# Kernel tuning notes

Hardware: AMD Instinct MI355X
Metric: run time of the kernel (lower is better)

Reference implementation:

```python
import jax, jax.numpy as jnp
import numpy as np

NUM_GRAPHS = 1024


def _mlp2(h, Wa, ba, Wb, bb):
    # Linear -> ReLU -> Linear
    return jax.nn.relu(h @ Wa + ba) @ Wb + bb


def setup_inputs() -> dict:
    key = jax.random.key(0)
    ks = jax.random.split(key, 16)
    N, F, H, C, E = 100000, 128, 128, 10, 1600000
    x = jax.random.normal(ks[0], (N, F), dtype=jnp.float32)
    edge_index = jax.random.randint(ks[1], (2, E), 0, N, dtype=jnp.int64)
    batch = jnp.sort(jax.random.randint(ks[2], (N,), 0, NUM_GRAPHS, dtype=jnp.int64))
    s = 1.0 / np.sqrt(H)
    def w(k, shape):
        return jax.random.uniform(k, shape, jnp.float32, -s, s)
    return {
        "x": x, "edge_index": edge_index, "batch": batch,
        "W1a": w(ks[3], (F, H)), "b1a": w(ks[4], (H,)),
        "W1b": w(ks[5], (H, H)), "b1b": w(ks[6], (H,)),
        "W2a": w(ks[7], (H, H)), "b2a": w(ks[8], (H,)),
        "W2b": w(ks[9], (H, H)), "b2b": w(ks[10], (H,)),
        "Wl1": w(ks[11], (H, H)), "bl1": w(ks[12], (H,)),
        "Wl2": w(ks[13], (H, C)), "bl2": w(ks[14], (C,)),
    }


def reference(x, edge_index, batch, W1a, b1a, W1b, b1b, W2a, b2a, W2b, b2b, Wl1, bl1, Wl2, bl2):
    N = x.shape[0]
    src, dst = edge_index[0], edge_index[1]

    def gin_conv(h, Wa, ba, Wb, bb):
        # sum-aggregate neighbor features: agg[i] = sum_{(src->dst=i)} h[src]
        agg = jax.ops.segment_sum(h[src], dst, num_segments=N)
        # eps = 0 (PyG default): nn((1+eps)*h + agg)
        return _mlp2(h + agg, Wa, ba, Wb, bb)

    h = jax.nn.relu(gin_conv(x, W1a, b1a, W1b, b1b))
    h = jax.nn.relu(gin_conv(h, W2a, b2a, W2b, b2b))
    # global_add_pool over graph ids -> [num_graphs, H]
    g = jax.ops.segment_sum(h, batch, num_segments=NUM_GRAPHS)
    g = jax.nn.relu(g @ Wl1 + bl1)
    return jax.nn.log_softmax(g @ Wl2 + bl2, axis=1)
```

## Files before the change

kernel.cpp:

```cpp
#include <hip/hip_runtime.h>
#include <hip/hip_bf16.h>
#include <math.h>

#define NUM_GRAPHS 1024

typedef __attribute__((ext_vector_type(8))) short bf16x8;
typedef __attribute__((ext_vector_type(4))) float f32x4;

static __device__ __forceinline__ unsigned short f2bf(float f) {
    union { float f; unsigned u; } v; v.f = f;
    unsigned r = v.u + 0x7fffu + ((v.u >> 16) & 1u);
    return (unsigned short)(r >> 16);
}
static __device__ __forceinline__ float bf_lo(unsigned u) { return __uint_as_float(u << 16); }
static __device__ __forceinline__ float bf_hi(unsigned u) { return __uint_as_float(u & 0xffff0000u); }

__global__ void k_pre(const int* __restrict__ eiDst, int E,
                      int* __restrict__ deg, int* __restrict__ rank,
                      const float* __restrict__ x, int n4, unsigned* __restrict__ xb,
                      float* __restrict__ G, int eb) {
    if ((int)blockIdx.x < eb) {
        int e = blockIdx.x * 256 + threadIdx.x;
        if (e < E) rank[e] = atomicAdd(&deg[eiDst[e]], 1);
    } else if ((int)blockIdx.x < eb + 4096) {
        int i = (blockIdx.x - eb) * 256 + threadIdx.x;
        int stride = 4096 * 256;
        const float4* x4 = (const float4*)x;
        for (; i < n4; i += stride) {
            float4 v = x4[i];
            unsigned lo = (unsigned)f2bf(v.x) | ((unsigned)f2bf(v.y) << 16);
            unsigned hi = (unsigned)f2bf(v.z) | ((unsigned)f2bf(v.w) << 16);
            ((uint2*)xb)[i] = make_uint2(lo, hi);
        }
    } else {
        int i = (blockIdx.x - eb - 4096) * 256 + threadIdx.x;
        float4* G4 = (float4*)G;
        for (; i < NUM_GRAPHS * 32; i += 64 * 256)
            G4[i] = make_float4(0.f, 0.f, 0.f, 0.f);
    }
}

__global__ void k_scan1(const int* __restrict__ deg, int N,
                        int* __restrict__ excl, int* __restrict__ bsum) {
    __shared__ int s[256];
    int i = blockIdx.x * 256 + threadIdx.x;
    int v = (i < N) ? deg[i] : 0;
    s[threadIdx.x] = v;
    __syncthreads();
    for (int off = 1; off < 256; off <<= 1) {
        int t = (threadIdx.x >= off) ? s[threadIdx.x - off] : 0;
        __syncthreads();
        s[threadIdx.x] += t;
        __syncthreads();
    }
    if (i < N) excl[i] = s[threadIdx.x] - v;
    if (threadIdx.x == 255) bsum[blockIdx.x] = s[255];
}

__global__ void k_scan23(const int* __restrict__ excl, const int* __restrict__ bsum,
                         int nb, int N, int E, int* __restrict__ rp) {
    __shared__ int s[512];
    const int t = threadIdx.x;
    for (int k = t; k < 512; k += 256) s[k] = (k < nb) ? bsum[k] : 0;
    __syncthreads();
    #pragma unroll
    for (int off = 1; off < 512; off <<= 1) {
        int a = (t >= off) ? s[t - off] : 0;
        int b = s[t + 256 - off];
        __syncthreads();
        s[t] += a;
        s[t + 256] += b;
        __syncthreads();
    }
    const int myIncl = s[blockIdx.x];
    const int myOwn = bsum[blockIdx.x];
    const int off_b = myIncl - myOwn;
    int i = blockIdx.x * 256 + t;
    if (i < N) rp[i] = excl[i] + off_b;
    if (i == 0) rp[N] = E;
}

#define FILL_PASSES 3
#define FILL_RANGE 33334
#define FILL_BLOCKS 2048
__global__ void k_fillprep(const int* __restrict__ ei, const int* __restrict__ rank,
                           int E, const int* __restrict__ rp, int* __restrict__ srcs,
                           const float* __restrict__ W0, const float* __restrict__ W1,
                           const float* __restrict__ W2, const float* __restrict__ W3,
                           unsigned short* __restrict__ wt) {
    if ((int)blockIdx.x < FILL_BLOCKS) {
        const int tid0 = blockIdx.x * 256 + threadIdx.x;
        const int stride = FILL_BLOCKS * 256;
        for (int pass = 0; pass < FILL_PASSES; ++pass) {
            const int lo = pass * FILL_RANGE;
            const int hi = lo + FILL_RANGE;
            for (int e = tid0; e < E; e += stride) {
                int d = ei[(size_t)E + e];
                if (d >= lo && d < hi) {
                    srcs[rp[d] + rank[e]] = ei[e];
                }
            }
        }
    } else {
        int lb = blockIdx.x - FILL_BLOCKS;
        int b = lb >> 6;
        const float* W = (b == 0) ? W0 : (b == 1) ? W1 : (b == 2) ? W2 : W3;
        int idx = (lb & 63) * 256 + threadIdx.x;
        int k = idx >> 7, n = idx & 127;
        wt[b * 16384 + n * 128 + k] = f2bf(W[idx]);
    }
}

__device__ __forceinline__ void acc8(float* a, uint4 v) {
    a[0] += bf_lo(v.x); a[1] += bf_hi(v.x);
    a[2] += bf_lo(v.y); a[3] += bf_hi(v.y);
    a[4] += bf_lo(v.z); a[5] += bf_hi(v.z);
    a[6] += bf_lo(v.w); a[7] += bf_hi(v.w);
}

__global__ __launch_bounds__(256, 8)
void k_aggq(const uint4* __restrict__ H4, const int* __restrict__ rp,
            const int* __restrict__ srcs, int N, uint4* __restrict__ out) {
    int gw = (blockIdx.x * blockDim.x + threadIdx.x) >> 6;
    int lane = threadIdx.x & 63;
    int q = lane >> 4, ql = lane & 15;
    int n = gw * 4 + q;
    if (gw * 4 >= N) return;
    bool act = (n < N);
    int nc = act ? n : 0;
    uint4 s0 = H4[(size_t)nc * 16 + ql];
    float a[8];
    a[0] = bf_lo(s0.x); a[1] = bf_hi(s0.x);
    a[2] = bf_lo(s0.y); a[3] = bf_hi(s0.y);
    a[4] = bf_lo(s0.z); a[5] = bf_hi(s0.z);
    a[6] = bf_lo(s0.w); a[7] = bf_hi(s0.w);
    int j = act ? rp[nc] : 0;
    int e = act ? rp[nc + 1] : 0;
    while (j + 4 <= e) {
        int i0 = srcs[j], i1 = srcs[j + 1], i2 = srcs[j + 2], i3 = srcs[j + 3];
        uint4 v0 = H4[(size_t)i0 * 16 + ql];
        uint4 v1 = H4[(size_t)i1 * 16 + ql];
        uint4 v2 = H4[(size_t)i2 * 16 + ql];
        uint4 v3 = H4[(size_t)i3 * 16 + ql];
        acc8(a, v0); acc8(a, v1); acc8(a, v2); acc8(a, v3);
        j += 4;
    }
    while (j < e) {
        uint4 v = H4[(size_t)srcs[j] * 16 + ql];
        acc8(a, v);
        ++j;
    }
    if (act) {
        uint4 o;
        o.x = (unsigned)f2bf(a[0]) | ((unsigned)f2bf(a[1]) << 16);
        o.y = (unsigned)f2bf(a[2]) | ((unsigned)f2bf(a[3]) << 16);
        o.z = (unsigned)f2bf(a[4]) | ((unsigned)f2bf(a[5]) << 16);
        o.w = (unsigned)f2bf(a[6]) | ((unsigned)f2bf(a[7]) << 16);
        out[(size_t)n * 16 + ql] = o;
    }
}

__device__ __forceinline__ int swz_base(int row, int chunk) {
    return row * 128 + ((chunk ^ (row & 7)) << 3);
}

template <bool POOL>
__global__ __launch_bounds__(256, 2)
void k_mlp(const unsigned short* __restrict__ U, int N,
           const unsigned short* __restrict__ WaT, const float* __restrict__ ba,
           const unsigned short* __restrict__ WbT, const float* __restrict__ bb,
           unsigned short* __restrict__ Y,
           const int* __restrict__ batch, float* __restrict__ G) {
    __shared__ unsigned short lA[128 * 128];
    __shared__ unsigned short lW[128 * 128];
    __shared__ int bs[128];

    const int tid = threadIdx.x;
    const int lane = tid & 63;
    const int w = tid >> 6;
    const int wr = (w >> 1) * 64;
    const int wc = (w & 1) * 64;
    const int r0 = blockIdx.x * 128;

    {
        const uint4* U4 = (const uint4*)U;
        #pragma unroll
        for (int i = 0; i < 8; ++i) {
            int c = tid + 256 * i;
            int row = c >> 4, q = c & 15;
            uint4 v = (r0 + row < N) ? U4[(size_t)(r0 + row) * 16 + q]
                                     : make_uint4(0u, 0u, 0u, 0u);
            *(uint4*)&lA[swz_base(row, q)] = v;
        }
    }
    {
        const uint4* Wsrc = (const uint4*)WaT;
        #pragma unroll
        for (int i = 0; i < 8; ++i) {
            int c = tid + 256 * i;
            int row = c >> 4, q = c & 15;
            *(uint4*)&lW[swz_base(row, q)] = Wsrc[c];
        }
    }
    __syncthreads();

    const int am = lane & 15;
    const int kq = (lane >> 4) * 8;

    f32x4 acc[4][4];
    #pragma unroll
    for (int i = 0; i < 4; ++i)
        #pragma unroll
        for (int j = 0; j < 4; ++j) acc[i][j] = (f32x4){0.f, 0.f, 0.f, 0.f};

    #pragma unroll
    for (int ks = 0; ks < 4; ++ks) {
        int k0 = ks * 32 + kq;
        bf16x8 af[4], bq[4];
        #pragma unroll
        for (int i = 0; i < 4; ++i)
            af[i] = *(const bf16x8*)&lA[swz_base(wr + i * 16 + am, k0 >> 3)];
        #pragma unroll
        for (int j = 0; j < 4; ++j)
            bq[j] = *(const bf16x8*)&lW[swz_base(wc + j * 16 + am, k0 >> 3)];
        #pragma unroll
        for (int i = 0; i < 4; ++i)
            #pragma unroll
            for (int j = 0; j < 4; ++j)
                acc[i][j] = __builtin_amdgcn_mfma_f32_16x16x32_bf16(af[i], bq[j], acc[i][j], 0, 0, 0);
    }
    __syncthreads();

    #pragma unroll
    for (int j = 0; j < 4; ++j) {
        int col = wc + j * 16 + am;
        float bias = ba[col];
        #pragma unroll
        for (int i = 0; i < 4; ++i) {
            int rowb = wr + i * 16 + (lane >> 4) * 4;
            #pragma unroll
            for (int r = 0; r < 4; ++r) {
                float t = acc[i][j][r] + bias;
                t = t > 0.f ? t : 0.f;
                int row = rowb + r;
                lA[swz_base(row, col >> 3) + (col & 7)] = f2bf(t);
            }
        }
    }
    {
        const uint4* Wsrc = (const uint4*)WbT;
        #pragma unroll
        for (int i = 0; i < 8; ++i) {
            int c = tid + 256 * i;
            int row = c >> 4, q = c & 15;
            *(uint4*)&lW[swz_base(row, q)] = Wsrc[c];
        }
    }
    __syncthreads();

    #pragma unroll
    for (int i = 0; i < 4; ++i)
        #pragma unroll
        for (int j = 0; j < 4; ++j) acc[i][j] = (f32x4){0.f, 0.f, 0.f, 0.f};

    #pragma unroll
    for (int ks = 0; ks < 4; ++ks) {
        int k0 = ks * 32 + kq;
        bf16x8 af[4], bq[4];
        #pragma unroll
        for (int i = 0; i < 4; ++i)
            af[i] = *(const bf16x8*)&lA[swz_base(wr + i * 16 + am, k0 >> 3)];
        #pragma unroll
        for (int j = 0; j < 4; ++j)
            bq[j] = *(const bf16x8*)&lW[swz_base(wc + j * 16 + am, k0 >> 3)];
        #pragma unroll
        for (int i = 0; i < 4; ++i)
            #pragma unroll
            for (int j = 0; j < 4; ++j)
                acc[i][j] = __builtin_amdgcn_mfma_f32_16x16x32_bf16(af[i], bq[j], acc[i][j], 0, 0, 0);
    }

    if (!POOL) {
        #pragma unroll
        for (int j = 0; j < 4; ++j) {
            int col = wc + j * 16 + am;
            float bias = bb[col];
            #pragma unroll
            for (int i = 0; i < 4; ++i) {
                int rowb = wr + i * 16 + (lane >> 4) * 4;
                #pragma unroll
                for (int r = 0; r < 4; ++r) {
                    int row = r0 + rowb + r;
                    if (row < N) {
                        float t = acc[i][j][r] + bias;
                        t = t > 0.f ? t : 0.f;
                        Y[(size_t)row * 128 + col] = f2bf(t);
                    }
                }
            }
        }
    } else {
        __syncthreads();
        #pragma unroll
        for (int j = 0; j < 4; ++j) {
            int col = wc + j * 16 + am;
            float bias = bb[col];
            #pragma unroll
            for (int i = 0; i < 4; ++i) {
                int rowb = wr + i * 16 + (lane >> 4) * 4;
                #pragma unroll
                for (int r = 0; r < 4; ++r) {
                    float t = acc[i][j][r] + bias;
                    t = t > 0.f ? t : 0.f;
                    int row = rowb + r;
                    lA[swz_base(row, col >> 3) + (col & 7)] = f2bf(t);
                }
            }
        }
        if (tid < 128) bs[tid] = (r0 + tid < N) ? batch[r0 + tid] : -1;
        __syncthreads();
        const int col = tid & 127;
        const int half = tid >> 7;
        const int rbeg = half * 64, rend = rbeg + 64;
        float pacc = 0.f;
        int cur = bs[rbeg];
        for (int row = rbeg; row < rend; ++row) {
            int b = bs[row];
            if (b != cur) {
                if (cur >= 0) atomicAdd(&G[(size_t)cur * 128 + col], pacc);
                pacc = 0.f;
                cur = b;
            }
            unsigned short u = lA[swz_base(row, col >> 3) + (col & 7)];
            pacc += __uint_as_float((unsigned)u << 16);
        }
        if (cur >= 0) atomicAdd(&G[(size_t)cur * 128 + col], pacc);
    }
}

__global__ void k_head(const float* __restrict__ G,
                       const float* __restrict__ Wl1, const float* __restrict__ bl1,
                       const float* __restrict__ Wl2, const float* __restrict__ bl2,
                       int C, float* __restrict__ out) {
    __shared__ float sg[128];
    __shared__ float sh[128];
    __shared__ float sl[16];
    int row = blockIdx.x;
    int t = threadIdx.x;
    sg[t] = G[(size_t)row * 128 + t];
    __syncthreads();
    float a = bl1[t];
    for (int k = 0; k < 128; ++k) a += sg[k] * Wl1[k * 128 + t];
    sh[t] = a > 0.f ? a : 0.f;
    __syncthreads();
    if (t < C) {
        float l = bl2[t];
        for (int k = 0; k < 128; ++k) l += sh[k] * Wl2[k * C + t];
        sl[t] = l;
    }
    __syncthreads();
    if (t < C) {
        float m = -1e30f;
        for (int j = 0; j < C; ++j) m = fmaxf(m, sl[j]);
        float s = 0.f;
        for (int j = 0; j < C; ++j) s += __expf(sl[j] - m);
        out[(size_t)row * C + t] = sl[t] - m - __logf(s);
    }
}

extern "C" void kernel_launch(void* const* d_in, const int* in_sizes, int n_in,
                              void* d_out, int out_size, void* d_ws, size_t ws_size,
                              hipStream_t stream) {
    const float* x    = (const float*)d_in[0];
    const int*   ei   = (const int*)d_in[1];
    const int*   batch= (const int*)d_in[2];
    const float* W1a  = (const float*)d_in[3];
    const float* b1a  = (const float*)d_in[4];
    const float* W1b  = (const float*)d_in[5];
    const float* b1b  = (const float*)d_in[6];
    const float* W2a  = (const float*)d_in[7];
    const float* b2a  = (const float*)d_in[8];
    const float* W2b  = (const float*)d_in[9];
    const float* b2b  = (const float*)d_in[10];
    const float* Wl1  = (const float*)d_in[11];
    const float* bl1  = (const float*)d_in[12];
    const float* Wl2  = (const float*)d_in[13];
    const float* bl2  = (const float*)d_in[14];
    float* out = (float*)d_out;

    const int N = in_sizes[2];
    const int E = in_sizes[1] / 2;
    const int C = in_sizes[13] / 128;

    char* p = (char*)d_ws;
    auto alloc = [&](size_t bytes) {
        char* r = p;
        p += (bytes + 255) & ~(size_t)255;
        return r;
    };
    unsigned* xb = (unsigned*)alloc((size_t)N * 64 * 4);
    unsigned* hA = (unsigned*)alloc((size_t)N * 64 * 4);
    unsigned* hB = (unsigned*)alloc((size_t)N * 64 * 4);
    float* g   = (float*)alloc((size_t)NUM_GRAPHS * 128 * 4);
    int* deg   = (int*)alloc((size_t)N * 4);
    int* excl  = (int*)alloc((size_t)N * 4);
    int* rp    = (int*)alloc((size_t)(N + 1) * 4);
    int* rank  = (int*)alloc((size_t)E * 4);
    int* bsum  = (int*)alloc(4096);
    int* srcs  = (int*)alloc((size_t)E * 4);
    unsigned short* wt = (unsigned short*)alloc((size_t)4 * 16384 * 2);
    (void)ws_size; (void)n_in; (void)out_size;

    const int nb = (N + 255) / 256;
    const int eb = (E + 255) / 256;

    hipMemsetAsync(deg, 0, (size_t)N * 4, stream);

    k_pre<<<eb + 4096 + 64, 256, 0, stream>>>(ei + E, E, deg, rank, x, N * 32, xb, g, eb);
    k_scan1<<<nb, 256, 0, stream>>>(deg, N, excl, bsum);
    k_scan23<<<nb, 256, 0, stream>>>(excl, bsum, nb, N, E, rp);
    k_fillprep<<<FILL_BLOCKS + 256, 256, 0, stream>>>(ei, rank, E, rp, srcs,
                                                      W1a, W1b, W2a, W2b, wt);

    const int mb = (N + 127) / 128;
    const int qw = (N + 3) / 4;
    const int qb = (qw + 3) / 4;

    k_aggq<<<qb, 256, 0, stream>>>((const uint4*)xb, rp, srcs, N, (uint4*)hA);
    k_mlp<false><<<mb, 256, 0, stream>>>((const unsigned short*)hA, N, wt, b1a,
                                         wt + 16384, b1b, (unsigned short*)hB,
                                         nullptr, nullptr);
    k_aggq<<<qb, 256, 0, stream>>>((const uint4*)hB, rp, srcs, N, (uint4*)hA);
    k_mlp<true><<<mb, 256, 0, stream>>>((const unsigned short*)hA, N, wt + 2 * 16384, b2a,
                                        wt + 3 * 16384, b2b, nullptr,
                                        batch, g);
    k_head<<<NUM_GRAPHS, 128, 0, stream>>>(g, Wl1, bl1, Wl2, bl2, C, out);
}
```

Measured before the change: 419.8 us.

## Replace global-atomic CSR build with two-level bucketed counting sort

Replaces the per-edge global atomic degree counting, the multi-pass range-filtered fill and the two scan kernels with a two-level radix-style counting sort. Edges are histogrammed into 128-node buckets using shared-memory atomics, then column-scanned, scattered into a packed bucket buffer, and finally sorted within each bucket to produce the row pointers and source indices. This removes contended global atomics and the three-pass rescan of all edges. In exchange it adds a serial per-bucket column scan over 512 entries, an extra packed edge buffer, and a redundant scan of the bucket totals in every block. The packing keeps the source index in the low 25 bits, which limits N to about 33 million nodes.

```diff
diff --git a/kernel.cpp b/kernel.cpp
--- a/kernel.cpp
+++ b/kernel.cpp
@@ -3,6 +3,7 @@
 #include <math.h>
 
 #define NUM_GRAPHS 1024
+#define NBLK 512
 
 typedef __attribute__((ext_vector_type(8))) short bf16x8;
 typedef __attribute__((ext_vector_type(4))) float f32x4;
@@ -15,16 +16,54 @@
 static __device__ __forceinline__ float bf_lo(unsigned u) { return __uint_as_float(u << 16); }
 static __device__ __forceinline__ float bf_hi(unsigned u) { return __uint_as_float(u & 0xffff0000u); }
 
-__global__ void k_pre(const int* __restrict__ eiDst, int E,
-                      int* __restrict__ deg, int* __restrict__ rank,
+static __device__ void scan_tot(const int* __restrict__ tot, int nbuck,
+                                int* bb, int* tmp) {
+    const int t = threadIdx.x;
+    int v[4];
+    int lsum = 0;
+    #pragma unroll
+    for (int j = 0; j < 4; ++j) {
+        int idx = 4 * t + j;
+        v[j] = (idx < nbuck) ? tot[idx] : 0;
+        lsum += v[j];
+    }
+    tmp[t] = lsum;
+    __syncthreads();
+    for (int off = 1; off < 256; off <<= 1) {
+        int a = (t >= off) ? tmp[t - off] : 0;
+        __syncthreads();
+        tmp[t] += a;
+        __syncthreads();
+    }
+    int run = tmp[t] - lsum;
+    #pragma unroll
+    for (int j = 0; j < 4; ++j) {
+        int idx = 4 * t + j;
+        if (idx < nbuck) bb[idx] = run;
+        run += v[j];
+    }
+    if (t == 255) bb[nbuck] = tmp[255];
+    __syncthreads();
+}
+
+__global__ void k_pre(const int* __restrict__ eiDst, int E, int epb, int nbuck,
+                      int* __restrict__ cnt,
                       const float* __restrict__ x, int n4, unsigned* __restrict__ xb,
-                      float* __restrict__ G, int eb) {
-    if ((int)blockIdx.x < eb) {
-        int e = blockIdx.x * 256 + threadIdx.x;
-        if (e < E) rank[e] = atomicAdd(&deg[eiDst[e]], 1);
-    } else if ((int)blockIdx.x < eb + 4096) {
-        int i = (blockIdx.x - eb) * 256 + threadIdx.x;
-        int stride = 4096 * 256;
+                      float* __restrict__ G) {
+    if ((int)blockIdx.x < NBLK) {
+        __shared__ int hist[1024];
+        const int t = threadIdx.x;
+        for (int i = t; i < 1024; i += 256) hist[i] = 0;
+        __syncthreads();
+        const int kb = blockIdx.x;
+        const int e0 = kb * epb;
+        const int e1 = min(E, e0 + epb);
+        for (int e = e0 + t; e < e1; e += 256) atomicAdd(&hist[eiDst[e] >> 7], 1);
+        __syncthreads();
+        for (int b = t; b < nbuck; b += 256) cnt[(size_t)b * NBLK + kb] = hist[b];
+    } else if ((int)blockIdx.x < NBLK + 2048) {
+        int i = (blockIdx.x - NBLK) * 256 + threadIdx.x;
+        const int stride = 2048 * 256;
         const float4* x4 = (const float4*)x;
         for (; i < n4; i += stride) {
             float4 v = x4[i];
@@ -33,81 +72,93 @@
             ((uint2*)xb)[i] = make_uint2(lo, hi);
         }
     } else {
-        int i = (blockIdx.x - eb - 4096) * 256 + threadIdx.x;
+        int i = (blockIdx.x - NBLK - 2048) * 256 + threadIdx.x;
         float4* G4 = (float4*)G;
         for (; i < NUM_GRAPHS * 32; i += 64 * 256)
             G4[i] = make_float4(0.f, 0.f, 0.f, 0.f);
     }
 }
 
-__global__ void k_scan1(const int* __restrict__ deg, int N,
-                        int* __restrict__ excl, int* __restrict__ bsum) {
-    __shared__ int s[256];
-    int i = blockIdx.x * 256 + threadIdx.x;
-    int v = (i < N) ? deg[i] : 0;
-    s[threadIdx.x] = v;
-    __syncthreads();
-    for (int off = 1; off < 256; off <<= 1) {
-        int t = (threadIdx.x >= off) ? s[threadIdx.x - off] : 0;
-        __syncthreads();
-        s[threadIdx.x] += t;
-        __syncthreads();
-    }
-    if (i < N) excl[i] = s[threadIdx.x] - v;
-    if (threadIdx.x == 255) bsum[blockIdx.x] = s[255];
-}
-
-__global__ void k_scan23(const int* __restrict__ excl, const int* __restrict__ bsum,
-                         int nb, int N, int E, int* __restrict__ rp) {
-    __shared__ int s[512];
+__global__ void k_colscan(const int* __restrict__ cnt, int nbuck,
+                          int* __restrict__ pref, int* __restrict__ tot) {
+    int b = blockIdx.x * 256 + threadIdx.x;
+    if (b >= nbuck) return;
+    const int* c = cnt + (size_t)b * NBLK;
+    int* pf = pref + (size_t)b * NBLK;
+    int run = 0;
+    #pragma unroll 4
+    for (int k = 0; k < NBLK; ++k) { pf[k] = run; run += c[k]; }
+    tot[b] = run;
+}
+
+__global__ void k_scatter(const int* __restrict__ eiSrc, const int* __restrict__ eiDst,
+                          int E, int epb, const int* __restrict__ pref,
+                          const int* __restrict__ tot, int nbuck,
+                          unsigned* __restrict__ ebuf) {
+    __shared__ int bb[1025];
+    __shared__ int tmp[256];
+    __shared__ int cur[1024];
     const int t = threadIdx.x;
-    for (int k = t; k < 512; k += 256) s[k] = (k < nb) ? bsum[k] : 0;
-    __syncthreads();
-    #pragma unroll
-    for (int off = 1; off < 512; off <<= 1) {
-        int a = (t >= off) ? s[t - off] : 0;
-        int b = s[t + 256 - off];
-        __syncthreads();
-        s[t] += a;
-        s[t + 256] += b;
-        __syncthreads();
-    }
-    const int myIncl = s[blockIdx.x];
-    const int myOwn = bsum[blockIdx.x];
-    const int off_b = myIncl - myOwn;
-    int i = blockIdx.x * 256 + t;
-    if (i < N) rp[i] = excl[i] + off_b;
-    if (i == 0) rp[N] = E;
-}
-
-#define FILL_PASSES 3
-#define FILL_RANGE 33334
-#define FILL_BLOCKS 2048
-__global__ void k_fillprep(const int* __restrict__ ei, const int* __restrict__ rank,
-                           int E, const int* __restrict__ rp, int* __restrict__ srcs,
-                           const float* __restrict__ W0, const float* __restrict__ W1,
-                           const float* __restrict__ W2, const float* __restrict__ W3,
-                           unsigned short* __restrict__ wt) {
-    if ((int)blockIdx.x < FILL_BLOCKS) {
-        const int tid0 = blockIdx.x * 256 + threadIdx.x;
-        const int stride = FILL_BLOCKS * 256;
-        for (int pass = 0; pass < FILL_PASSES; ++pass) {
-            const int lo = pass * FILL_RANGE;
-            const int hi = lo + FILL_RANGE;
-            for (int e = tid0; e < E; e += stride) {
-                int d = ei[(size_t)E + e];
-                if (d >= lo && d < hi) {
-                    srcs[rp[d] + rank[e]] = ei[e];
-                }
-            }
-        }
-    } else {
-        int lb = blockIdx.x - FILL_BLOCKS;
-        int b = lb >> 6;
-        const float* W = (b == 0) ? W0 : (b == 1) ? W1 : (b == 2) ? W2 : W3;
+    const int kb = blockIdx.x;
+    scan_tot(tot, nbuck, bb, tmp);
+    for (int b = t; b < nbuck; b += 256) cur[b] = bb[b] + pref[(size_t)b * NBLK + kb];
+    __syncthreads();
+    const int e0 = kb * epb;
+    const int e1 = min(E, e0 + epb);
+    for (int e = e0 + t; e < e1; e += 256) {
+        int d = eiDst[e];
+        int s = eiSrc[e];
+        int pos = atomicAdd(&cur[d >> 7], 1);
+        ebuf[pos] = (unsigned)s | ((unsigned)(d & 127) << 25);
+    }
+}
+
+__global__ void k_bucket(const unsigned* __restrict__ ebuf, const int* __restrict__ tot,
+                         int nbuck, int N, int* __restrict__ rp, int* __restrict__ srcs,
+                         const float* __restrict__ W0, const float* __restrict__ W1,
+                         const float* __restrict__ W2, const float* __restrict__ W3,
+                         unsigned short* __restrict__ wt) {
+    if ((int)blockIdx.x >= nbuck) {
+        int lb = blockIdx.x - nbuck;
+        int b4 = lb >> 6;
+        const float* W = (b4 == 0) ? W0 : (b4 == 1) ? W1 : (b4 == 2) ? W2 : W3;
         int idx = (lb & 63) * 256 + threadIdx.x;
         int k = idx >> 7, n = idx & 127;
-        wt[b * 16384 + n * 128 + k] = f2bf(W[idx]);
+        wt[b4 * 16384 + n * 128 + k] = f2bf(W[idx]);
+        return;
+    }
+    __shared__ int bb[1025];
+    __shared__ int tmp[256];
+    __shared__ int h[128];
+    __shared__ int cur[128];
+    const int t = threadIdx.x;
+    const int b = blockIdx.x;
+    scan_tot(tot, nbuck, bb, tmp);
+    const int base = bb[b];
+    const int cntb = bb[b + 1] - base;
+    if (t < 128) h[t] = 0;
+    __syncthreads();
+    for (int i = t; i < cntb; i += 256) atomicAdd(&h[ebuf[base + i] >> 25], 1);
+    __syncthreads();
+    int c0 = (t < 128) ? h[t] : 0;
+    for (int off = 1; off < 128; off <<= 1) {
+        int a = (t >= off && t < 128) ? h[t - off] : 0;
+        __syncthreads();
+        if (t < 128) h[t] += a;
+        __syncthreads();
+    }
+    if (t < 128) {
+        int excl = h[t] - c0;
+        cur[t] = excl;
+        int d = (b << 7) + t;
+        if (d < N) rp[d] = base + excl;
+        if (d == N) rp[N] = base + excl;
+    }
+    __syncthreads();
+    for (int i = t; i < cntb; i += 256) {
+        unsigned pck = ebuf[base + i];
+        int pos = atomicAdd(&cur[pck >> 25], 1);
+        srcs[base + pos] = (int)(pck & 0x01FFFFFFu);
     }
 }
 
@@ -392,35 +443,34 @@
     const int E = in_sizes[1] / 2;
     const int C = in_sizes[13] / 128;
 
+    const int nbuck = (N >> 7) + 1;
+    const int epb = (E + NBLK - 1) / NBLK;
+
     char* p = (char*)d_ws;
     auto alloc = [&](size_t bytes) {
         char* r = p;
         p += (bytes + 255) & ~(size_t)255;
         return r;
     };
-    unsigned* xb = (unsigned*)alloc((size_t)N * 64 * 4);
-    unsigned* hA = (unsigned*)alloc((size_t)N * 64 * 4);
-    unsigned* hB = (unsigned*)alloc((size_t)N * 64 * 4);
-    float* g   = (float*)alloc((size_t)NUM_GRAPHS * 128 * 4);
-    int* deg   = (int*)alloc((size_t)N * 4);
-    int* excl  = (int*)alloc((size_t)N * 4);
-    int* rp    = (int*)alloc((size_t)(N + 1) * 4);
-    int* rank  = (int*)alloc((size_t)E * 4);
-    int* bsum  = (int*)alloc(4096);
-    int* srcs  = (int*)alloc((size_t)E * 4);
+    unsigned* xb   = (unsigned*)alloc((size_t)N * 64 * 4);
+    unsigned* hA   = (unsigned*)alloc((size_t)N * 64 * 4);
+    unsigned* hB   = (unsigned*)alloc((size_t)N * 64 * 4);
+    float* g       = (float*)alloc((size_t)NUM_GRAPHS * 128 * 4);
+    int* rp        = (int*)alloc((size_t)(N + 1) * 4);
+    int* srcs      = (int*)alloc((size_t)E * 4);
+    unsigned* ebuf = (unsigned*)alloc((size_t)E * 4);
+    int* cnt       = (int*)alloc((size_t)nbuck * NBLK * 4);
+    int* pref      = (int*)alloc((size_t)nbuck * NBLK * 4);
+    int* tot       = (int*)alloc((size_t)1024 * 4);
     unsigned short* wt = (unsigned short*)alloc((size_t)4 * 16384 * 2);
     (void)ws_size; (void)n_in; (void)out_size;
 
-    const int nb = (N + 255) / 256;
-    const int eb = (E + 255) / 256;
-
-    hipMemsetAsync(deg, 0, (size_t)N * 4, stream);
-
-    k_pre<<<eb + 4096 + 64, 256, 0, stream>>>(ei + E, E, deg, rank, x, N * 32, xb, g, eb);
-    k_scan1<<<nb, 256, 0, stream>>>(deg, N, excl, bsum);
-    k_scan23<<<nb, 256, 0, stream>>>(excl, bsum, nb, N, E, rp);
-    k_fillprep<<<FILL_BLOCKS + 256, 256, 0, stream>>>(ei, rank, E, rp, srcs,
-                                                      W1a, W1b, W2a, W2b, wt);
+    k_pre<<<NBLK + 2048 + 64, 256, 0, stream>>>(ei + E, E, epb, nbuck, cnt,
+                                                x, N * 32, xb, g);
+    k_colscan<<<(nbuck + 255) / 256, 256, 0, stream>>>(cnt, nbuck, pref, tot);
+    k_scatter<<<NBLK, 256, 0, stream>>>(ei, ei + E, E, epb, pref, tot, nbuck, ebuf);
+    k_bucket<<<nbuck + 256, 256, 0, stream>>>(ebuf, tot, nbuck, N, rp, srcs,
+                                              W1a, W1b, W2a, W2b, wt);
 
     const int mb = (N + 127) / 128;
     const int qw = (N + 3) / 4;
```

Result: no change. 411.9 us (-1.9%).
